# Kernel optimization log

Hardware: AMD Instinct MI355X
Metric: run time of the kernel (lower is better)

## Reference

```python
import jax, jax.numpy as jnp
import numpy as np

H = 4096       # hidden_size
NH = 32        # num attention heads
DN = 128       # qk_nope_head_dim
DR = 64        # qk_rope_head_dim
DV = 128       # v_head_dim
QL = 1536      # q_lora_rank
KL = 512       # kv_lora_rank
INH = 32       # indexer heads
IHD = 128      # indexer head_dim (== fp8 quant block -> one scale per head)
TOPK = 512     # index_topk
T = 1024       # prefill tokens
SCALING = (DN + DR) ** -0.5
FP8_MAX = 448.0  # e4m3 max


def _rms(x, w, eps=1e-6):
    return x * jax.lax.rsqrt(jnp.mean(x * x, -1, keepdims=True) + eps) * w


def _ln(x, w, b, eps=1e-6):
    m = jnp.mean(x, -1, keepdims=True)
    v = jnp.mean(jnp.square(x - m), -1, keepdims=True)
    return (x - m) * jax.lax.rsqrt(v + eps) * w + b


def _rope(x, pos):
    # interleaved (non-neox) rotary embedding on the last dim
    d = x.shape[-1]
    inv = 1.0 / (10000.0 ** (jnp.arange(0, d, 2, dtype=jnp.float32) / d))
    ang = pos.astype(jnp.float32)[:, None] * inv  # [T, d/2]
    shape = (x.shape[0],) + (1,) * (x.ndim - 2) + (d // 2,)
    cos = jnp.cos(ang).reshape(shape)
    sin = jnp.sin(ang).reshape(shape)
    x1, x2 = x[..., 0::2], x[..., 1::2]
    return jnp.stack([x1 * cos - x2 * sin, x1 * sin + x2 * cos], -1).reshape(x.shape)


def _forward(hidden_states, w_qkv_a, q_a_ln_w, w_q_b, kv_a_ln_w, w_kv_b, w_o,
             w_idx_qb, w_idx_k, idx_k_ln_w, idx_k_ln_b, w_idx_weights, positions):
    Tq = hidden_states.shape[0]
    neg = jnp.finfo(jnp.float32).min
    # --- fused low-rank QKV-a projection ---
    qkv_a = hidden_states @ w_qkv_a                       # [T, QL+KL+DR]
    q_c, kv_c, k_pe = qkv_a[:, :QL], qkv_a[:, QL:QL + KL], qkv_a[:, QL + KL:]
    q_cn = _rms(q_c, q_a_ln_w)                            # qr (normed q latent)
    # --- MLA decompression ---
    q = (q_cn @ w_q_b).reshape(Tq, NH, DN + DR)
    q_nope, q_pe = q[..., :DN], q[..., DN:]
    kv = (_rms(kv_c, kv_a_ln_w) @ w_kv_b).reshape(Tq, NH, DN + DV)
    k_nope, v = kv[..., :DN], kv[..., DN:]
    q_pe = _rope(q_pe, positions)
    k_pe = _rope(k_pe, positions)                         # [T, DR], shared across heads (MQA)
    # --- lightning indexer (fp8 ue8m0 per-token-group quant emulated in fp32) ---
    qi = (q_cn @ w_idx_qb).reshape(Tq, INH, IHD)
    qi = jnp.concatenate([_rope(qi[..., :DR], positions), qi[..., DR:]], -1)
    ki = _ln(hidden_states @ w_idx_k, idx_k_ln_w, idx_k_ln_b)   # [T, IHD]
    ki = jnp.concatenate([_rope(ki[:, :DR], positions), ki[:, DR:]], -1)
    amax = jnp.max(jnp.abs(qi), -1, keepdims=True)        # group == head (IHD == block 128)
    q_scale = jnp.exp2(jnp.ceil(jnp.log2(jnp.maximum(amax, 1e-10) / FP8_MAX)))  # ue8m0
    qi_q = qi / q_scale                                   # values in fp8 range
    wts = (hidden_states @ w_idx_weights) * q_scale[..., 0]
    wts = wts * (IHD ** -0.5) * (INH ** -0.5)             # [T, INH]
    sim = jax.nn.relu(jnp.einsum('qhd,kd->hqk', qi_q, ki))
    logits = jnp.einsum('qh,hqk->qk', wts, sim)           # [Tq, Tk]
    idx = jnp.arange(Tq)
    causal = idx[:, None] >= idx[None, :]
    logits = jnp.where(causal, logits, neg)
    _, topk_idx = jax.lax.top_k(logits, TOPK)             # [T, TOPK]
    sparse_mask = jnp.zeros((Tq, Tq), bool).at[idx[:, None], topk_idx].set(True) & causal
    # --- sparse MLA attention ---
    qf = jnp.concatenate([q_nope, q_pe], -1)              # [T, NH, DN+DR]
    kf = jnp.concatenate([k_nope, jnp.broadcast_to(k_pe[:, None, :], (Tq, NH, DR))], -1)
    scores = jnp.einsum('qhd,khd->hqk', qf, kf) * SCALING
    scores = jnp.where(sparse_mask[None], scores, neg)
    attn = jax.nn.softmax(scores, -1)
    out = jnp.einsum('hqk,khd->qhd', attn, v).reshape(Tq, NH * DV)
    return out @ w_o                                      # [T, H]


def setup_inputs() -> dict:
    key = jax.random.key(0)
    ks = jax.random.split(key, 8)
    s = 0.02
    return {
        'hidden_states': jax.random.normal(ks[0], (T, H), jnp.float32),
        'positions': jnp.arange(T, dtype=jnp.int32),
        'w_qkv_a': jax.random.normal(ks[1], (H, QL + KL + DR), jnp.float32) * s,
        'q_a_ln_w': jnp.ones((QL,), jnp.float32),
        'w_q_b': jax.random.normal(ks[2], (QL, NH * (DN + DR)), jnp.float32) * s,
        'kv_a_ln_w': jnp.ones((KL,), jnp.float32),
        'w_kv_b': jax.random.normal(ks[3], (KL, NH * (DN + DV)), jnp.float32) * s,
        'w_o': jax.random.normal(ks[4], (NH * DV, H), jnp.float32) * s,
        'w_idx_qb': jax.random.normal(ks[5], (QL, INH * IHD), jnp.float32) * s,
        'w_idx_k': jax.random.normal(ks[6], (H, IHD), jnp.float32) * s,
        'idx_k_ln_w': jnp.ones((IHD,), jnp.float32),
        'idx_k_ln_b': jnp.zeros((IHD,), jnp.float32),
        'w_idx_weights': jax.random.normal(ks[7], (H, INH), jnp.float32) * s,
    }


def reference(hidden_states, positions, w_qkv_a, q_a_ln_w, w_q_b, kv_a_ln_w, w_kv_b, w_o,
              w_idx_qb, w_idx_k, idx_k_ln_w, idx_k_ln_b, w_idx_weights):
    return _forward(hidden_states, w_qkv_a, q_a_ln_w, w_q_b, kv_a_ln_w, w_kv_b, w_o,
                    w_idx_qb, w_idx_k, idx_k_ln_w, idx_k_ln_b, w_idx_weights, positions)
```

## Files before the change

kernel.cpp:

```cpp
#include <hip/hip_runtime.h>
#include <hip/hip_bf16.h>
#include <math.h>
#include <type_traits>

#define TT   1024
#define HH   4096
#define NHH  32
#define DNN  128
#define DRR  64
#define DVV  128
#define QLL  1536
#define KLL  512
#define INHH 32
#define IHDD 128
#define TOPKK 512
#define QKVN 2112

typedef __attribute__((ext_vector_type(8))) short short8;
typedef __attribute__((ext_vector_type(4))) short short4v;
typedef __attribute__((ext_vector_type(4))) float f32x4;

static __device__ __constant__ float kScaling = 0.07216878364870322f;
static __device__ __constant__ float kWtsScale = 0.015625f;

static __device__ __forceinline__ short f2bf(float f) {
  unsigned u = __float_as_uint(f);
  unsigned r = (u + 0x7fffu + ((u >> 16) & 1u)) >> 16;
  return (short)r;
}
static __device__ __forceinline__ float bf2f(short s) {
  return __uint_as_float(((unsigned)(unsigned short)s) << 16);
}
static __device__ __forceinline__ void gl16(const void* g, void* l) {
  __builtin_amdgcn_global_load_lds(
      (const __attribute__((address_space(1))) unsigned int*)g,
      (__attribute__((address_space(3))) unsigned int*)l, 16, 0, 0);
}
static __device__ __forceinline__ int xcd_swz(int n, int nwg) {
  const int q = nwg >> 3, r = nwg & 7;
  const int x = n & 7, i = n >> 3;
  return (x < r ? x * (q + 1) : r * (q + 1) + (x - r) * q) + i;
}

template <typename CT>
__global__ __launch_bounds__(256) void gemm_bf16(const short* __restrict__ A,
                                                 const short* __restrict__ Bt,
                                                 CT* __restrict__ C,
                                                 int M, int N, int K) {
  __shared__ short As[64 * 64];
  __shared__ short Bs[128 * 64];
  int flat = blockIdx.x + gridDim.x * blockIdx.y;
  flat = xcd_swz(flat, gridDim.x * gridDim.y);
  const int byg = flat % gridDim.y;
  const int bxg = flat / gridDim.y;
  const int tid = threadIdx.x;
  const int lane = tid & 63, wv = tid >> 6;
  const int wc = wv * 32;
  const int bm = byg * 64, bn = bxg * 128;
  const int l15 = lane & 15, l4 = lane >> 4;
  const int sx = (l15 & 7) * 8;
  f32x4 acc[4][2];
#pragma unroll
  for (int i = 0; i < 4; ++i)
#pragma unroll
    for (int j = 0; j < 2; ++j) acc[i][j] = f32x4{0.f, 0.f, 0.f, 0.f};
  for (int k0 = 0; k0 < K; k0 += 64) {
    __syncthreads();
#pragma unroll
    for (int i = 0; i < 2; ++i) {
      const int idx = tid + i * 256;
      const int row = idx >> 3, c8 = (idx & 7) * 8;
      const int cs = c8 ^ ((row & 7) * 8);
      gl16(A + (size_t)(bm + row) * K + k0 + cs, &As[idx * 8]);
    }
#pragma unroll
    for (int i = 0; i < 4; ++i) {
      const int idx = tid + i * 256;
      const int row = idx >> 3, c8 = (idx & 7) * 8;
      const int cs = c8 ^ ((row & 7) * 8);
      gl16(Bt + (size_t)(bn + row) * K + k0 + cs, &Bs[idx * 8]);
    }
    __syncthreads();
    short8 fa[4][2], fb[2][2];
#pragma unroll
    for (int rt = 0; rt < 4; ++rt)
#pragma unroll
      for (int kk = 0; kk < 2; ++kk)
        fa[rt][kk] = *(const short8*)(&As[(rt * 16 + l15) * 64 + ((kk * 32 + l4 * 8) ^ sx)]);
#pragma unroll
    for (int ct = 0; ct < 2; ++ct)
#pragma unroll
      for (int kk = 0; kk < 2; ++kk)
        fb[ct][kk] = *(const short8*)(&Bs[(wc + ct * 16 + l15) * 64 + ((kk * 32 + l4 * 8) ^ sx)]);
#pragma unroll
    for (int kk = 0; kk < 2; ++kk)
#pragma unroll
      for (int rt = 0; rt < 4; ++rt)
#pragma unroll
        for (int ct = 0; ct < 2; ++ct)
          acc[rt][ct] = __builtin_amdgcn_mfma_f32_16x16x32_bf16(fa[rt][kk], fb[ct][kk], acc[rt][ct], 0, 0, 0);
  }
#pragma unroll
  for (int rt = 0; rt < 4; ++rt)
#pragma unroll
    for (int ct = 0; ct < 2; ++ct)
#pragma unroll
      for (int r = 0; r < 4; ++r) {
        const int row = bm + rt * 16 + l4 * 4 + r;
        const int col = bn + wc + ct * 16 + l15;
        const float v = acc[rt][ct][r];
        if constexpr (std::is_same<CT, float>::value) C[(size_t)row * N + col] = v;
        else C[(size_t)row * N + col] = __float2bfloat16(v);
      }
}

__global__ __launch_bounds__(256) void gemm_qb(const short* __restrict__ A,
                                               const short* __restrict__ Bt,
                                               const int* __restrict__ pos,
                                               short* __restrict__ qhb) {
  const int M = TT, N = 6144, K = QLL;
  __shared__ short As[64 * 64];
  __shared__ short Bs[128 * 64];
  int flat = blockIdx.x + gridDim.x * blockIdx.y;
  flat = xcd_swz(flat, gridDim.x * gridDim.y);
  const int byg = flat % gridDim.y;
  const int bxg = flat / gridDim.y;
  const int tid = threadIdx.x;
  const int lane = tid & 63, wv = tid >> 6;
  const int wc = wv * 32;
  const int bm = byg * 64, bn = bxg * 128;
  const int l15 = lane & 15, l4 = lane >> 4;
  const int sx = (l15 & 7) * 8;
  f32x4 acc[4][2];
#pragma unroll
  for (int i = 0; i < 4; ++i)
#pragma unroll
    for (int j = 0; j < 2; ++j) acc[i][j] = f32x4{0.f, 0.f, 0.f, 0.f};
  for (int k0 = 0; k0 < K; k0 += 64) {
    __syncthreads();
#pragma unroll
    for (int i = 0; i < 2; ++i) {
      const int idx = tid + i * 256;
      const int row = idx >> 3, c8 = (idx & 7) * 8;
      const int cs = c8 ^ ((row & 7) * 8);
      gl16(A + (size_t)(bm + row) * K + k0 + cs, &As[idx * 8]);
    }
#pragma unroll
    for (int i = 0; i < 4; ++i) {
      const int idx = tid + i * 256;
      const int row = idx >> 3, c8 = (idx & 7) * 8;
      const int cs = c8 ^ ((row & 7) * 8);
      gl16(Bt + (size_t)(bn + row) * K + k0 + cs, &Bs[idx * 8]);
    }
    __syncthreads();
    short8 fa[4][2], fb[2][2];
#pragma unroll
    for (int rt = 0; rt < 4; ++rt)
#pragma unroll
      for (int kk = 0; kk < 2; ++kk)
        fa[rt][kk] = *(const short8*)(&As[(rt * 16 + l15) * 64 + ((kk * 32 + l4 * 8) ^ sx)]);
#pragma unroll
    for (int ct = 0; ct < 2; ++ct)
#pragma unroll
      for (int kk = 0; kk < 2; ++kk)
        fb[ct][kk] = *(const short8*)(&Bs[(wc + ct * 16 + l15) * 64 + ((kk * 32 + l4 * 8) ^ sx)]);
#pragma unroll
    for (int kk = 0; kk < 2; ++kk)
#pragma unroll
      for (int rt = 0; rt < 4; ++rt)
#pragma unroll
        for (int ct = 0; ct < 2; ++ct)
          acc[rt][ct] = __builtin_amdgcn_mfma_f32_16x16x32_bf16(fa[rt][kk], fb[ct][kk], acc[rt][ct], 0, 0, 0);
  }
#pragma unroll
  for (int rt = 0; rt < 4; ++rt)
#pragma unroll
    for (int r = 0; r < 4; ++r) {
      const int row = bm + rt * 16 + l4 * 4 + r;
      const float p = (float)pos[row];
#pragma unroll
      for (int ct = 0; ct < 2; ++ct) {
        const int col = bn + wc + ct * 16 + l15;
        float v = acc[rt][ct][r];
        const float pv = __shfl_xor(v, 1);
        const int head = col / 192, d = col - head * 192;
        if (d >= 128) {
          const int i = (d - 128) >> 1;
          const float inv = powf(10000.f, -(float)i * (1.f / 32.f));
          float sn, cs;
          sincosf(p * inv, &sn, &cs);
          v = (col & 1) ? (pv * sn + v * cs) : (v * cs - pv * sn);
        }
        qhb[((size_t)head * 1024 + row) * 192 + d] = f2bf(v);
      }
    }
}

__global__ __launch_bounds__(256) void gemm_kvb(const short* __restrict__ A,
                                                const short* __restrict__ Bt,
                                                short* __restrict__ kfb,
                                                short* __restrict__ vtb) {
  const int K = KLL;
  __shared__ short As[64 * 64];
  __shared__ short Bs[128 * 64];
  __shared__ short tr[128 * 66];
  int flat = blockIdx.x + gridDim.x * blockIdx.y;
  flat = xcd_swz(flat, gridDim.x * gridDim.y);
  const int byg = flat % gridDim.y;
  const int bxg = flat / gridDim.y;
  const int tid = threadIdx.x;
  const int lane = tid & 63, wv = tid >> 6;
  const int wc = wv * 32;
  const int bm = byg * 64, bn = bxg * 128;
  const int l15 = lane & 15, l4 = lane >> 4;
  const int sx = (l15 & 7) * 8;
  f32x4 acc[4][2];
#pragma unroll
  for (int i = 0; i < 4; ++i)
#pragma unroll
    for (int j = 0; j < 2; ++j) acc[i][j] = f32x4{0.f, 0.f, 0.f, 0.f};
  for (int k0 = 0; k0 < K; k0 += 64) {
    __syncthreads();
#pragma unroll
    for (int i = 0; i < 2; ++i) {
      const int idx = tid + i * 256;
      const int row = idx >> 3, c8 = (idx & 7) * 8;
      const int cs = c8 ^ ((row & 7) * 8);
      gl16(A + (size_t)(bm + row) * K + k0 + cs, &As[idx * 8]);
    }
#pragma unroll
    for (int i = 0; i < 4; ++i) {
      const int idx = tid + i * 256;
      const int row = idx >> 3, c8 = (idx & 7) * 8;
      const int cs = c8 ^ ((row & 7) * 8);
      gl16(Bt + (size_t)(bn + row) * K + k0 + cs, &Bs[idx * 8]);
    }
    __syncthreads();
    short8 fa[4][2], fb[2][2];
#pragma unroll
    for (int rt = 0; rt < 4; ++rt)
#pragma unroll
      for (int kk = 0; kk < 2; ++kk)
        fa[rt][kk] = *(const short8*)(&As[(rt * 16 + l15) * 64 + ((kk * 32 + l4 * 8) ^ sx)]);
#pragma unroll
    for (int ct = 0; ct < 2; ++ct)
#pragma unroll
      for (int kk = 0; kk < 2; ++kk)
        fb[ct][kk] = *(const short8*)(&Bs[(wc + ct * 16 + l15) * 64 + ((kk * 32 + l4 * 8) ^ sx)]);
#pragma unroll
    for (int kk = 0; kk < 2; ++kk)
#pragma unroll
      for (int rt = 0; rt < 4; ++rt)
#pragma unroll
        for (int ct = 0; ct < 2; ++ct)
          acc[rt][ct] = __builtin_amdgcn_mfma_f32_16x16x32_bf16(fa[rt][kk], fb[ct][kk], acc[rt][ct], 0, 0, 0);
  }
  const int h = bn >> 8;
  const bool isv = (bn >> 7) & 1;
  if (!isv) {
#pragma unroll
    for (int rt = 0; rt < 4; ++rt)
#pragma unroll
      for (int ct = 0; ct < 2; ++ct)
#pragma unroll
        for (int r = 0; r < 4; ++r) {
          const int row = bm + rt * 16 + l4 * 4 + r;
          const int d = wc + ct * 16 + l15;
          kfb[((size_t)h * 1024 + row) * 192 + d] = f2bf(acc[rt][ct][r]);
        }
  } else {
    __syncthreads();
#pragma unroll
    for (int rt = 0; rt < 4; ++rt)
#pragma unroll
      for (int ct = 0; ct < 2; ++ct)
#pragma unroll
        for (int r = 0; r < 4; ++r)
          tr[(wc + ct * 16 + l15) * 66 + rt * 16 + l4 * 4 + r] = f2bf(acc[rt][ct][r]);
    __syncthreads();
    const int d = tid >> 1, half = tid & 1;
    short* dst = vtb + ((size_t)h * 128 + d) * 1024 + bm + half * 32;
#pragma unroll
    for (int c = 0; c < 4; ++c) {
      short8 o;
#pragma unroll
      for (int e = 0; e < 8; ++e) o[e] = tr[d * 66 + half * 32 + c * 8 + e];
      *(short8*)(dst + c * 8) = o;
    }
  }
}

__global__ __launch_bounds__(256) void gemm1_splitk(const short* __restrict__ A,
                                                    const short* __restrict__ Bt,
                                                    float* __restrict__ part,
                                                    int M, int Np, int K, int kchunk) {
  __shared__ short As[64 * 64];
  __shared__ short Bs[128 * 64];
  int flat = blockIdx.x + gridDim.x * (blockIdx.y + gridDim.y * blockIdx.z);
  flat = xcd_swz(flat, gridDim.x * gridDim.y * gridDim.z);
  const int byg = flat % gridDim.y;
  int tmp = flat / gridDim.y;
  const int bxg = tmp % gridDim.x, bzg = tmp / gridDim.x;
  const int tid = threadIdx.x;
  const int lane = tid & 63, wv = tid >> 6;
  const int wc = wv * 32;
  const int bm = byg * 64, bn = bxg * 128;
  const int kbeg = bzg * kchunk;
  const int l15 = lane & 15, l4 = lane >> 4;
  const int sx = (l15 & 7) * 8;
  f32x4 acc[4][2];
#pragma unroll
  for (int i = 0; i < 4; ++i)
#pragma unroll
    for (int j = 0; j < 2; ++j) acc[i][j] = f32x4{0.f, 0.f, 0.f, 0.f};
  for (int k0 = kbeg; k0 < kbeg + kchunk; k0 += 64) {
    __syncthreads();
#pragma unroll
    for (int i = 0; i < 2; ++i) {
      const int idx = tid + i * 256;
      const int row = idx >> 3, c8 = (idx & 7) * 8;
      const int cs = c8 ^ ((row & 7) * 8);
      gl16(A + (size_t)(bm + row) * K + k0 + cs, &As[idx * 8]);
    }
#pragma unroll
    for (int i = 0; i < 4; ++i) {
      const int idx = tid + i * 256;
      const int row = idx >> 3, c8 = (idx & 7) * 8;
      const int cs = c8 ^ ((row & 7) * 8);
      gl16(Bt + (size_t)(bn + row) * K + k0 + cs, &Bs[idx * 8]);
    }
    __syncthreads();
    short8 fa[4][2], fb[2][2];
#pragma unroll
    for (int rt = 0; rt < 4; ++rt)
#pragma unroll
      for (int kk = 0; kk < 2; ++kk)
        fa[rt][kk] = *(const short8*)(&As[(rt * 16 + l15) * 64 + ((kk * 32 + l4 * 8) ^ sx)]);
#pragma unroll
    for (int ct = 0; ct < 2; ++ct)
#pragma unroll
      for (int kk = 0; kk < 2; ++kk)
        fb[ct][kk] = *(const short8*)(&Bs[(wc + ct * 16 + l15) * 64 + ((kk * 32 + l4 * 8) ^ sx)]);
#pragma unroll
    for (int kk = 0; kk < 2; ++kk)
#pragma unroll
      for (int rt = 0; rt < 4; ++rt)
#pragma unroll
        for (int ct = 0; ct < 2; ++ct)
          acc[rt][ct] = __builtin_amdgcn_mfma_f32_16x16x32_bf16(fa[rt][kk], fb[ct][kk], acc[rt][ct], 0, 0, 0);
  }
  float* dst = part + (size_t)bzg * M * Np;
#pragma unroll
  for (int rt = 0; rt < 4; ++rt)
#pragma unroll
    for (int ct = 0; ct < 2; ++ct)
#pragma unroll
      for (int r = 0; r < 4; ++r)
        dst[(size_t)(bm + rt * 16 + l4 * 4 + r) * Np + bn + wc + ct * 16 + l15] =
            acc[rt][ct][r];
}

__global__ __launch_bounds__(256) void gemm3(const short* __restrict__ Ah,
                                             const short* __restrict__ Al,
                                             const short* __restrict__ Bth,
                                             const short* __restrict__ Btl,
                                             float* __restrict__ part,
                                             int M, int Np, int K, int kchunk) {
  __shared__ short AS[64 * 64], BS[128 * 64];
  int flat = blockIdx.x + gridDim.x * (blockIdx.y + gridDim.y * blockIdx.z);
  flat = xcd_swz(flat, gridDim.x * gridDim.y * gridDim.z);
  const int byg = flat % gridDim.y;
  int tmp = flat / gridDim.y;
  const int bxg = tmp % gridDim.x, bzg = tmp / gridDim.x;
  const int tid = threadIdx.x;
  const int lane = tid & 63, wv = tid >> 6;
  const int wc = wv * 32;
  const int l15 = lane & 15, l4 = lane >> 4;
  const int sx = (l15 & 7) * 8;
  const int bm = byg * 64, bn = bxg * 128;
  const int kbeg = bzg * kchunk;
  f32x4 acc[4][2];
#pragma unroll
  for (int i = 0; i < 4; ++i)
#pragma unroll
    for (int j = 0; j < 2; ++j) acc[i][j] = f32x4{0.f, 0.f, 0.f, 0.f};
  for (int k0 = kbeg; k0 < kbeg + kchunk; k0 += 32) {
    __syncthreads();
#pragma unroll
    for (int i = 0; i < 2; ++i) {
      const int idx = tid + i * 256;
      const int row = idx >> 3, c8 = (idx & 7) * 8;
      const int cs = c8 ^ ((row & 7) * 8);
      const short* srcA = (cs < 32) ? (Ah + (size_t)(bm + row) * K + k0 + cs)
                                    : (Al + (size_t)(bm + row) * K + k0 + (cs - 32));
      gl16(srcA, &AS[idx * 8]);
    }
#pragma unroll
    for (int i = 0; i < 4; ++i) {
      const int idx = tid + i * 256;
      const int row = idx >> 3, c8 = (idx & 7) * 8;
      const int cs = c8 ^ ((row & 7) * 8);
      const short* srcB = (cs < 32) ? (Bth + (size_t)(bn + row) * K + k0 + cs)
                                    : (Btl + (size_t)(bn + row) * K + k0 + (cs - 32));
      gl16(srcB, &BS[idx * 8]);
    }
    __syncthreads();
    short8 fah[4], fal[4], fbh[2], fbl[2];
#pragma unroll
    for (int rt = 0; rt < 4; ++rt) {
      const int row = rt * 16 + l15;
      fah[rt] = *(const short8*)&AS[row * 64 + ((l4 * 8) ^ sx)];
      fal[rt] = *(const short8*)&AS[row * 64 + ((32 + l4 * 8) ^ sx)];
    }
#pragma unroll
    for (int ct = 0; ct < 2; ++ct) {
      const int row = wc + ct * 16 + l15;
      fbh[ct] = *(const short8*)&BS[row * 64 + ((l4 * 8) ^ sx)];
      fbl[ct] = *(const short8*)&BS[row * 64 + ((32 + l4 * 8) ^ sx)];
    }
#pragma unroll
    for (int ct = 0; ct < 2; ++ct)
#pragma unroll
      for (int rt = 0; rt < 4; ++rt) {
        acc[rt][ct] = __builtin_amdgcn_mfma_f32_16x16x32_bf16(fah[rt], fbh[ct], acc[rt][ct], 0, 0, 0);
        acc[rt][ct] = __builtin_amdgcn_mfma_f32_16x16x32_bf16(fah[rt], fbl[ct], acc[rt][ct], 0, 0, 0);
        acc[rt][ct] = __builtin_amdgcn_mfma_f32_16x16x32_bf16(fal[rt], fbh[ct], acc[rt][ct], 0, 0, 0);
      }
  }
  float* dst = part + (size_t)bzg * M * Np;
#pragma unroll
  for (int rt = 0; rt < 4; ++rt)
#pragma unroll
    for (int ct = 0; ct < 2; ++ct)
#pragma unroll
      for (int r = 0; r < 4; ++r)
        dst[(size_t)(bm + rt * 16 + l4 * 4 + r) * Np + bn + wc + ct * 16 + l15] =
            acc[rt][ct][r];
}

__global__ __launch_bounds__(256) void qkv_post(const float* __restrict__ qpart,
                                                const float* __restrict__ tpart,
                                                const float* __restrict__ q_ln_w,
                                                const float* __restrict__ kv_ln_w,
                                                const int* __restrict__ pos,
                                                short* __restrict__ qcn_bf,
                                                short* __restrict__ qcn_lo,
                                                short* __restrict__ kvn_bf,
                                                short* __restrict__ kpe_bf) {
  const int t = blockIdx.x, tid = threadIdx.x;
  __shared__ float red[4];
  float qv[6];
  float ss = 0.f;
#pragma unroll
  for (int j = 0; j < 6; ++j) {
    const int c = tid + j * 256;
    float s = 0.f;
#pragma unroll
    for (int z = 0; z < 4; ++z) s += qpart[((size_t)z * TT + t) * QLL + c];
    qv[j] = s;
    ss = fmaf(s, s, ss);
  }
#pragma unroll
  for (int o = 32; o > 0; o >>= 1) ss += __shfl_xor(ss, o);
  if ((tid & 63) == 0) red[tid >> 6] = ss;
  __syncthreads();
  const float rq = rsqrtf((red[0] + red[1] + red[2] + red[3]) / (float)QLL + 1e-6f);
  __syncthreads();
#pragma unroll
  for (int j = 0; j < 6; ++j) {
    const int c = tid + j * 256;
    const float v = qv[j] * rq * q_ln_w[c];
    const short h = f2bf(v);
    qcn_bf[(size_t)t * QLL + c] = h;
    qcn_lo[(size_t)t * QLL + c] = f2bf(v - bf2f(h));
  }
  float kv2[2];
  float ss2 = 0.f;
#pragma unroll
  for (int j = 0; j < 2; ++j) {
    const int c = tid + j * 256;
    float s = 0.f;
#pragma unroll
    for (int z = 0; z < 4; ++z) s += tpart[((size_t)z * TT + t) * 640 + c];
    kv2[j] = s;
    ss2 = fmaf(s, s, ss2);
  }
#pragma unroll
  for (int o = 32; o > 0; o >>= 1) ss2 += __shfl_xor(ss2, o);
  if ((tid & 63) == 0) red[tid >> 6] = ss2;
  __syncthreads();
  const float rkv = rsqrtf((red[0] + red[1] + red[2] + red[3]) / (float)KLL + 1e-6f);
#pragma unroll
  for (int j = 0; j < 2; ++j) {
    const int c = tid + j * 256;
    kvn_bf[(size_t)t * KLL + c] = f2bf(kv2[j] * rkv * kv_ln_w[c]);
  }
  if (tid < 32) {
    float x1 = 0.f, x2 = 0.f;
#pragma unroll
    for (int z = 0; z < 4; ++z) {
      x1 += tpart[((size_t)z * TT + t) * 640 + 512 + 2 * tid];
      x2 += tpart[((size_t)z * TT + t) * 640 + 512 + 2 * tid + 1];
    }
    const float inv = powf(10000.f, -(float)tid * (1.f / 32.f));
    float sn, cs;
    sincosf((float)pos[t] * inv, &sn, &cs);
    kpe_bf[(size_t)t * 64 + 2 * tid]     = f2bf(x1 * cs - x2 * sn);
    kpe_bf[(size_t)t * 64 + 2 * tid + 1] = f2bf(x1 * sn + x2 * cs);
  }
}

__global__ __launch_bounds__(256) void kpe_fill(const short* __restrict__ kpe_bf,
                                                short* __restrict__ kfb) {
  const int idx = blockIdx.x * 256 + threadIdx.x;
  const int c = idx & 7, k = (idx >> 3) & 1023, h = idx >> 13;
  short8 v = *(const short8*)(kpe_bf + k * 64 + c * 8);
  *(short8*)(kfb + ((size_t)h * 1024 + k) * 192 + 128 + c * 8) = v;
}

__global__ __launch_bounds__(256) void ki_prep2(const float* __restrict__ part,
                                                const float* __restrict__ w,
                                                const float* __restrict__ b,
                                                const int* __restrict__ pos,
                                                short* __restrict__ kih,
                                                short* __restrict__ kil,
                                                float* __restrict__ wtsb) {
  const int t = blockIdx.x, tid = threadIdx.x;
  __shared__ float red[4], red2[4];
  float s = 0.f;
#pragma unroll
  for (int z = 0; z < 8; ++z) s += part[((size_t)z * TT + t) * 256 + tid];
  if (tid >= 128 && tid < 160) wtsb[(size_t)t * 32 + (tid - 128)] = s;
  const float v = (tid < 128) ? s : 0.f;
  float sm = v;
#pragma unroll
  for (int o = 32; o > 0; o >>= 1) sm += __shfl_xor(sm, o);
  if ((tid & 63) == 0) red[tid >> 6] = sm;
  __syncthreads();
  const float m = (red[0] + red[1]) * (1.f / 128.f);
  const float dv = v - m;
  float sq = (tid < 128) ? dv * dv : 0.f;
#pragma unroll
  for (int o = 32; o > 0; o >>= 1) sq += __shfl_xor(sq, o);
  if ((tid & 63) == 0) red2[tid >> 6] = sq;
  __syncthreads();
  const float var = (red2[0] + red2[1]) * (1.f / 128.f);
  if (tid < 128) {
    float x = dv * rsqrtf(var + 1e-6f) * w[tid] + b[tid];
    if (tid < 64) {
      const float part2 = __shfl_xor(x, 1);
      const int pi = tid >> 1;
      const float inv = powf(10000.f, -(float)pi * (1.f / 32.f));
      float sn, cs;
      sincosf((float)pos[t] * inv, &sn, &cs);
      x = (tid & 1) ? (part2 * sn + x * cs) : (x * cs - part2 * sn);
    }
    const short h = f2bf(x);
    kih[(size_t)t * 128 + tid] = h;
    kil[(size_t)t * 128 + tid] = f2bf(x - bf2f(h));
  }
}

__global__ __launch_bounds__(256) void split_cast(const float* __restrict__ in,
                                                  short* __restrict__ hi,
                                                  short* __restrict__ lo, int n4) {
  const int i = blockIdx.x * 256 + threadIdx.x;
  if (i >= n4) return;
  float4 v = *(const float4*)(in + (size_t)i * 4);
  float av[4] = {v.x, v.y, v.z, v.w};
  short4v h, l;
#pragma unroll
  for (int e = 0; e < 4; ++e) {
    h[e] = f2bf(av[e]);
    l[e] = f2bf(av[e] - bf2f(h[e]));
  }
  *(short4v*)(hi + (size_t)i * 4) = h;
  *(short4v*)(lo + (size_t)i * 4) = l;
}

__global__ __launch_bounds__(256) void transpose_cast_g(const float* __restrict__ B,
                                                        short* __restrict__ Bt,
                                                        int K, int ldB, int col0, int Ncols) {
  __shared__ float tile[64][65];
  const int tid = threadIdx.x;
  const int k0 = blockIdx.y * 64, n0 = blockIdx.x * 64;
  const int nl = tid >> 3, kc = (tid & 7) * 8;
  if (n0 >= Ncols) {
    short8 z = {0, 0, 0, 0, 0, 0, 0, 0};
#pragma unroll
    for (int i = 0; i < 2; ++i) {
      const int n = nl + i * 32;
      *(short8*)(Bt + (size_t)(n0 + n) * K + k0 + kc) = z;
    }
    return;
  }
  const int r = tid >> 4, c4 = (tid & 15) * 4;
#pragma unroll
  for (int i = 0; i < 4; ++i) {
    float4 v = *(const float4*)(B + (size_t)(k0 + r + i * 16) * ldB + col0 + n0 + c4);
    tile[r + i * 16][c4 + 0] = v.x;
    tile[r + i * 16][c4 + 1] = v.y;
    tile[r + i * 16][c4 + 2] = v.z;
    tile[r + i * 16][c4 + 3] = v.w;
  }
  __syncthreads();
#pragma unroll
  for (int i = 0; i < 2; ++i) {
    const int n = nl + i * 32;
    short8 o;
#pragma unroll
    for (int e = 0; e < 8; ++e) o[e] = f2bf(tile[kc + e][n]);
    *(short8*)(Bt + (size_t)(n0 + n) * K + k0 + kc) = o;
  }
}

__global__ __launch_bounds__(256) void transpose_split_cast(const float* __restrict__ B,
                                                            short* __restrict__ Bth,
                                                            short* __restrict__ Btl,
                                                            int K, int ldB, int col0,
                                                            int Ncols) {
  __shared__ float tile[64][65];
  const int tid = threadIdx.x;
  const int k0 = blockIdx.y * 64, n0 = blockIdx.x * 64;
  const int nl = tid >> 3, kc = (tid & 7) * 8;
  if (n0 >= Ncols) {
    short8 z = {0, 0, 0, 0, 0, 0, 0, 0};
#pragma unroll
    for (int i = 0; i < 2; ++i) {
      const int n = nl + i * 32;
      *(short8*)(Bth + (size_t)(n0 + n) * K + k0 + kc) = z;
      *(short8*)(Btl + (size_t)(n0 + n) * K + k0 + kc) = z;
    }
    return;
  }
  const int r = tid >> 4, c4 = (tid & 15) * 4;
#pragma unroll
  for (int i = 0; i < 4; ++i) {
    float4 v = make_float4(0.f, 0.f, 0.f, 0.f);
    if (n0 + c4 < Ncols)
      v = *(const float4*)(B + (size_t)(k0 + r + i * 16) * ldB + col0 + n0 + c4);
    tile[r + i * 16][c4 + 0] = v.x;
    tile[r + i * 16][c4 + 1] = v.y;
    tile[r + i * 16][c4 + 2] = v.z;
    tile[r + i * 16][c4 + 3] = v.w;
  }
  __syncthreads();
#pragma unroll
  for (int i = 0; i < 2; ++i) {
    const int n = nl + i * 32;
    short8 oh, ol;
#pragma unroll
    for (int e = 0; e < 8; ++e) {
      const float x = tile[kc + e][n];
      oh[e] = f2bf(x);
      ol[e] = f2bf(x - bf2f(oh[e]));
    }
    *(short8*)(Bth + (size_t)(n0 + n) * K + k0 + kc) = oh;
    *(short8*)(Btl + (size_t)(n0 + n) * K + k0 + kc) = ol;
  }
}

__global__ __launch_bounds__(256) void qi_rope_repack_split(const float* __restrict__ idxpart,
                                                            const int* __restrict__ pos,
                                                            short* __restrict__ qhh,
                                                            short* __restrict__ qhl) {
  const int qt = blockIdx.x, h = blockIdx.y;
  const int tid = threadIdx.x;
  const size_t plane = (size_t)TT * HH;
#pragma unroll
  for (int i = 0; i < 8; ++i) {
    const int idx = tid + i * 256;
    const int q = idx >> 5, c = idx & 31;
    const int qg = qt * 64 + q;
    const size_t base = (size_t)qg * HH + h * 128 + c * 4;
    float4 v0 = *(const float4*)(idxpart + base);
    float4 v1 = *(const float4*)(idxpart + plane + base);
    float av[4] = {v0.x + v1.x, v0.y + v1.y, v0.z + v1.z, v0.w + v1.w};
    if (c < 16) {
      const float p = (float)pos[qg];
      float sn0, cs0, sn1, cs1;
      sincosf(p * powf(10000.f, -(float)(c * 2) * (1.f / 32.f)), &sn0, &cs0);
      sincosf(p * powf(10000.f, -(float)(c * 2 + 1) * (1.f / 32.f)), &sn1, &cs1);
      const float a0 = av[0] * cs0 - av[1] * sn0, a1 = av[0] * sn0 + av[1] * cs0;
      const float a2 = av[2] * cs1 - av[3] * sn1, a3 = av[2] * sn1 + av[3] * cs1;
      av[0] = a0; av[1] = a1; av[2] = a2; av[3] = a3;
    }
    short4v hv, lv;
#pragma unroll
    for (int e = 0; e < 4; ++e) {
      hv[e] = f2bf(av[e]);
      lv[e] = f2bf(av[e] - bf2f(hv[e]));
    }
    const size_t off = ((size_t)h * 1024 + qt * 64 + q) * 128 + c * 4;
    *(short4v*)(qhh + off) = hv;
    *(short4v*)(qhl + off) = lv;
  }
}

__global__ __launch_bounds__(256) void logits_mfma(const short* __restrict__ qih,
                                                   const short* __restrict__ qil,
                                                   const short* __restrict__ kih_g,
                                                   const short* __restrict__ kil_g,
                                                   const float* __restrict__ wts,
                                                   float* __restrict__ part) {
  const int bid = xcd_swz(blockIdx.x, gridDim.x);
  int bq = (int)((sqrtf(8.f * bid + 1.f) - 1.f) * 0.5f);
  while ((bq + 1) * (bq + 2) / 2 <= bid) ++bq;
  while (bq * (bq + 1) / 2 > bid) --bq;
  const int bk = bid - bq * (bq + 1) / 2;
  const int g = blockIdx.y;
  __shared__ short kih[64 * 128], kil[64 * 128];
  __shared__ float swts[64][8];
  const int tid = threadIdx.x;
  const int lane = tid & 63, wv = tid >> 6;
  const int wr = (wv >> 1) * 32, wc = (wv & 1) * 32;
  const int l15 = lane & 15, l4 = lane >> 4;
  const int q0 = bq * 64, k0 = bk * 64;
  {
    const int r0 = tid >> 4;
    const int c8 = (tid & 15) * 8;
#pragma unroll
    for (int i = 0; i < 4; ++i) {
      const int row = r0 + i * 16;
      gl16(kih_g + (size_t)(k0 + row) * 128 + c8, &kih[(tid + i * 256) * 8]);
      gl16(kil_g + (size_t)(k0 + row) * 128 + c8, &kil[(tid + i * 256) * 8]);
    }
  }
#pragma unroll
  for (int i = 0; i < 2; ++i) {
    const int idx = tid + i * 256;
    swts[idx >> 3][idx & 7] = wts[(size_t)(q0 + (idx >> 3)) * 32 + g * 8 + (idx & 7)];
  }
  __syncthreads();
  short8 kbh[2][4], kbl[2][4];
#pragma unroll
  for (int ct = 0; ct < 2; ++ct)
#pragma unroll
    for (int ks = 0; ks < 4; ++ks) {
      kbh[ct][ks] = *(const short8*)&kih[(wc + ct * 16 + l15) * 128 + ks * 32 + l4 * 8];
      kbl[ct][ks] = *(const short8*)&kil[(wc + ct * 16 + l15) * 128 + ks * 32 + l4 * 8];
    }
  f32x4 lacc[2][2];
#pragma unroll
  for (int i = 0; i < 2; ++i)
#pragma unroll
    for (int j = 0; j < 2; ++j) lacc[i][j] = f32x4{0.f, 0.f, 0.f, 0.f};
  for (int hh = 0; hh < 8; ++hh) {
    const int h = g * 8 + hh;
    short8 qah[2][4], qal[2][4];
#pragma unroll
    for (int rt = 0; rt < 2; ++rt)
#pragma unroll
      for (int ks = 0; ks < 4; ++ks) {
        const size_t off = ((size_t)h * 1024 + q0 + wr + rt * 16 + l15) * 128 + ks * 32 + l4 * 8;
        qah[rt][ks] = *(const short8*)(qih + off);
        qal[rt][ks] = *(const short8*)(qil + off);
      }
    f32x4 hacc[2][2];
#pragma unroll
    for (int i = 0; i < 2; ++i)
#pragma unroll
      for (int j = 0; j < 2; ++j) hacc[i][j] = f32x4{0.f, 0.f, 0.f, 0.f};
#pragma unroll
    for (int ks = 0; ks < 4; ++ks)
#pragma unroll
      for (int rt = 0; rt < 2; ++rt)
#pragma unroll
        for (int ct = 0; ct < 2; ++ct) {
          hacc[rt][ct] = __builtin_amdgcn_mfma_f32_16x16x32_bf16(qah[rt][ks], kbh[ct][ks], hacc[rt][ct], 0, 0, 0);
          hacc[rt][ct] = __builtin_amdgcn_mfma_f32_16x16x32_bf16(qah[rt][ks], kbl[ct][ks], hacc[rt][ct], 0, 0, 0);
          hacc[rt][ct] = __builtin_amdgcn_mfma_f32_16x16x32_bf16(qal[rt][ks], kbh[ct][ks], hacc[rt][ct], 0, 0, 0);
        }
#pragma unroll
    for (int rt = 0; rt < 2; ++rt)
#pragma unroll
      for (int ct = 0; ct < 2; ++ct)
#pragma unroll
        for (int r = 0; r < 4; ++r) {
          const int row = wr + rt * 16 + l4 * 4 + r;
          const float w = swts[row][hh] * kWtsScale;
          lacc[rt][ct][r] = fmaf(w, fmaxf(hacc[rt][ct][r], 0.f), lacc[rt][ct][r]);
        }
  }
#pragma unroll
  for (int rt = 0; rt < 2; ++rt)
#pragma unroll
    for (int ct = 0; ct < 2; ++ct)
#pragma unroll
      for (int r = 0; r < 4; ++r)
        part[(size_t)g * TT * TT + (size_t)(q0 + wr + rt * 16 + l4 * 4 + r) * TT +
             (k0 + wc + ct * 16 + l15)] = lacc[rt][ct][r];
}

__global__ __launch_bounds__(256) void topk_mask(const float* __restrict__ part,
                                                 unsigned* __restrict__ maskbuf) {
  const int w = threadIdx.x >> 6;
  const int lane = threadIdx.x & 63;
  const int q = blockIdx.x * 4 + w;
  const size_t NN = (size_t)TT * TT;
  __shared__ unsigned long long bl[4][16];
  unsigned v[16];
#pragma unroll
  for (int j = 0; j < 16; ++j) {
    const int k = j * 64 + lane;
    unsigned uv = 0u;
    if (k <= q) {
      const size_t o = (size_t)q * TT + k;
      const float s = part[o] + part[NN + o] + part[2 * NN + o] + part[3 * NN + o];
      unsigned bb = __float_as_uint(s);
      uv = (bb & 0x80000000u) ? ~bb : (bb | 0x80000000u);
    }
    v[j] = uv;
  }
  if (q + 1 <= TOPKK) {
#pragma unroll
    for (int j = 0; j < 16; ++j) {
      const unsigned long long m = __ballot(j * 64 + lane <= q);
      if (lane == 0) bl[w][j] = m;
    }
  } else {
    unsigned lo = 1u, hi = 0xFFFFFFFFu;
    while (lo < hi) {
      const unsigned mid = lo + ((hi - lo) >> 1) + ((hi - lo) & 1u);
      int c = 0;
#pragma unroll
      for (int j = 0; j < 16; ++j) c += __popcll(__ballot(v[j] >= mid));
      if (c >= TOPKK) lo = mid; else hi = mid - 1u;
    }
    const unsigned ustar = lo;
    int nGreater = 0;
#pragma unroll
    for (int j = 0; j < 16; ++j) nGreater += __popcll(__ballot(v[j] > ustar));
    int need = TOPKK - nGreater;
    const unsigned long long lanemask = lane ? (~0ull >> (64 - lane)) : 0ull;
#pragma unroll
    for (int j = 0; j < 16; ++j) {
      const unsigned long long bg = __ballot(v[j] > ustar);
      const unsigned long long be = __ballot(v[j] == ustar);
      const int ce = __popcll(be);
      const int take = need < ce ? need : ce;
      const int rank = __popcll(be & lanemask);
      const bool selme = ((be >> lane) & 1ull) && (rank < take);
      const unsigned long long m = bg | __ballot(selme);
      if (lane == 0) bl[w][j] = m;
      need -= take;
    }
  }
  __builtin_amdgcn_s_waitcnt(0);
  if (lane < 32)
    maskbuf[(size_t)q * 32 + lane] = (unsigned)(bl[w][lane >> 1] >> ((lane & 1) * 32));
}

__global__ __launch_bounds__(256) void attn_mfma(const short* __restrict__ qh,
                                                 const short* __restrict__ kf,
                                                 const short* __restrict__ vt,
                                                 const unsigned* __restrict__ maskbuf,
                                                 short* __restrict__ ao) {
  const int h = blockIdx.x;
  const int yy = blockIdx.y;
  const int qt = (yy < 8) ? (yy * 2) : (31 - yy * 2);
  const int tid = threadIdx.x;
  const int lane = tid & 63, w = tid >> 6;
  const int l15 = lane & 15, l4 = lane >> 4;
  const int q0 = qt * 64;
  __shared__ short kfs[64 * 200];
  __shared__ short vts[128 * 72];
  __shared__ short ps[4][16][72];
  __shared__ unsigned m32s[64][2];
  short8 qf[6];
#pragma unroll
  for (int ks = 0; ks < 6; ++ks)
    qf[ks] = *(const short8*)(qh + ((size_t)h * 1024 + q0 + w * 16 + l15) * 192 + ks * 32 + l4 * 8);
  f32x4 of[8];
#pragma unroll
  for (int dt = 0; dt < 8; ++dt) of[dt] = f32x4{0.f, 0.f, 0.f, 0.f};
  float m[4], l[4];
#pragma unroll
  for (int r = 0; r < 4; ++r) { m[r] = -INFINITY; l[r] = 0.f; }

  for (int kt = 0; kt <= qt; ++kt) {
    const int k0 = kt * 64;
    __syncthreads();
#pragma unroll
    for (int i = 0; i < 6; ++i) {
      const int idx = tid + i * 256;
      const int row = idx / 24, c = idx - row * 24;
      *(short8*)&kfs[row * 200 + c * 8] =
          *(const short8*)(kf + ((size_t)h * 1024 + k0 + row) * 192 + c * 8);
    }
#pragma unroll
    for (int i = 0; i < 4; ++i) {
      const int idx = tid + i * 256;
      const int row = idx >> 3, c = idx & 7;
      *(short8*)&vts[row * 72 + c * 8] =
          *(const short8*)(vt + ((size_t)h * 128 + row) * 1024 + k0 + c * 8);
    }
    if (tid < 128)
      m32s[tid >> 1][tid & 1] = maskbuf[(size_t)(q0 + (tid >> 1)) * 32 + (k0 >> 5) + (tid & 1)];
    __syncthreads();
    f32x4 sacc[4];
#pragma unroll
    for (int j = 0; j < 4; ++j) sacc[j] = f32x4{0.f, 0.f, 0.f, 0.f};
#pragma unroll
    for (int ks = 0; ks < 6; ++ks)
#pragma unroll
      for (int j = 0; j < 4; ++j) {
        short8 kb = *(const short8*)&kfs[(j * 16 + l15) * 200 + ks * 32 + l4 * 8];
        sacc[j] = __builtin_amdgcn_mfma_f32_16x16x32_bf16(qf[ks], kb, sacc[j], 0, 0, 0);
      }
    float tmax[4] = {-INFINITY, -INFINITY, -INFINITY, -INFINITY};
#pragma unroll
    for (int j = 0; j < 4; ++j)
#pragma unroll
      for (int r = 0; r < 4; ++r) {
        const int kcol = j * 16 + l15;
        const unsigned um = m32s[w * 16 + l4 * 4 + r][kcol >> 5];
        float s = sacc[j][r] * kScaling;
        s = ((um >> (kcol & 31)) & 1u) ? s : -INFINITY;
        sacc[j][r] = s;
        tmax[r] = fmaxf(tmax[r], s);
      }
#pragma unroll
    for (int r = 0; r < 4; ++r) {
      tmax[r] = fmaxf(tmax[r], __shfl_xor(tmax[r], 1));
      tmax[r] = fmaxf(tmax[r], __shfl_xor(tmax[r], 2));
      tmax[r] = fmaxf(tmax[r], __shfl_xor(tmax[r], 4));
      tmax[r] = fmaxf(tmax[r], __shfl_xor(tmax[r], 8));
    }
    float f[4];
#pragma unroll
    for (int r = 0; r < 4; ++r) {
      const float mn = fmaxf(m[r], tmax[r]);
      f[r] = __expf(fmaxf(m[r], -1e30f) - fmaxf(mn, -1e30f));
      m[r] = mn;
      l[r] *= f[r];
    }
    float psum[4] = {0.f, 0.f, 0.f, 0.f};
#pragma unroll
    for (int j = 0; j < 4; ++j)
#pragma unroll
      for (int r = 0; r < 4; ++r) {
        const float p = __expf(sacc[j][r] - fmaxf(m[r], -1e30f));
        psum[r] += p;
        ps[w][l4 * 4 + r][j * 16 + l15] = f2bf(p);
      }
#pragma unroll
    for (int r = 0; r < 4; ++r) {
      psum[r] += __shfl_xor(psum[r], 1);
      psum[r] += __shfl_xor(psum[r], 2);
      psum[r] += __shfl_xor(psum[r], 4);
      psum[r] += __shfl_xor(psum[r], 8);
      l[r] += psum[r];
    }
#pragma unroll
    for (int dt = 0; dt < 8; ++dt)
#pragma unroll
      for (int r = 0; r < 4; ++r) of[dt][r] *= f[r];
    short8 pa0 = *(const short8*)&ps[w][l15][l4 * 8];
    short8 pa1 = *(const short8*)&ps[w][l15][32 + l4 * 8];
#pragma unroll
    for (int dt = 0; dt < 8; ++dt) {
      short8 vb0 = *(const short8*)&vts[(dt * 16 + l15) * 72 + l4 * 8];
      short8 vb1 = *(const short8*)&vts[(dt * 16 + l15) * 72 + 32 + l4 * 8];
      of[dt] = __builtin_amdgcn_mfma_f32_16x16x32_bf16(pa0, vb0, of[dt], 0, 0, 0);
      of[dt] = __builtin_amdgcn_mfma_f32_16x16x32_bf16(pa1, vb1, of[dt], 0, 0, 0);
    }
  }
#pragma unroll
  for (int r = 0; r < 4; ++r) {
    const float invl = 1.f / l[r];
#pragma unroll
    for (int dt = 0; dt < 8; ++dt)
      ao[(size_t)(q0 + w * 16 + l4 * 4 + r) * 4096 + h * 128 + dt * 16 + l15] =
          f2bf(of[dt][r] * invl);
  }
}

extern "C" void kernel_launch(void* const* d_in, const int* in_sizes, int n_in,
                              void* d_out, int out_size, void* d_ws, size_t ws_size,
                              hipStream_t stream) {
  const float* hidden     = (const float*)d_in[0];
  const int*   positions  = (const int*)d_in[1];
  const float* w_qkv_a    = (const float*)d_in[2];
  const float* q_a_ln_w   = (const float*)d_in[3];
  const float* w_q_b      = (const float*)d_in[4];
  const float* kv_a_ln_w  = (const float*)d_in[5];
  const float* w_kv_b     = (const float*)d_in[6];
  const float* w_o        = (const float*)d_in[7];
  const float* w_idx_qb   = (const float*)d_in[8];
  const float* w_idx_k    = (const float*)d_in[9];
  const float* idx_k_ln_w = (const float*)d_in[10];
  const float* idx_k_ln_b = (const float*)d_in[11];
  const float* w_idx_w    = (const float*)d_in[12];
  float* out = (float*)d_out;

  float* ws = (float*)d_ws;
  size_t off = 0;
  auto take = [&](size_t n) { float* p = ws + off; off += n; return p; };
  short* qcn_bf  = (short*)take((size_t)TT * QLL / 2);
  short* qcn_lo  = (short*)take((size_t)TT * QLL / 2);
  short* kvn_bf  = (short*)take((size_t)TT * KLL / 2);
  short* kpe_bf  = (short*)take((size_t)TT * 32);
  float* wtsb    = take((size_t)TT * INHH);
  short* kih_g   = (short*)take((size_t)TT * IHDD / 2);
  short* kil_g   = (short*)take((size_t)TT * IHDD / 2);
  short* qhb     = (short*)take((size_t)NHH * TT * 192 / 2);
  short* kfb     = (short*)take((size_t)NHH * TT * 192 / 2);
  short* vtb     = (short*)take((size_t)NHH * 128 * TT / 2);
  short* qih_h   = (short*)take((size_t)INHH * TT * 128 / 2);
  short* qih_l   = (short*)take((size_t)INHH * TT * 128 / 2);
  float* part4   = take((size_t)4 * TT * TT);
  unsigned* maskbuf = (unsigned*)take((size_t)TT * 32);
  short* hid_h   = (short*)take((size_t)TT * HH / 2);
  short* hid_l   = (short*)take((size_t)TT * HH / 2);
  short* wqkva_h = (short*)take((size_t)QLL * HH / 2);
  short* wqkva_l = (short*)take((size_t)QLL * HH / 2);
  short* wtail_t = (short*)take((size_t)640 * HH / 2);
  short* wsk_h   = (short*)take((size_t)256 * HH / 2);
  short* wsk_l   = (short*)take((size_t)256 * HH / 2);
  short* widxqb_h = (short*)take((size_t)HH * QLL / 2);
  short* widxqb_l = (short*)take((size_t)HH * QLL / 2);
  short* wqb_t   = (short*)take((size_t)6144 * QLL / 2);
  short* wkvb_t  = (short*)take((size_t)8192 * KLL / 2);
  short* ao   = (short*)part4;
  short* wo_t = hid_h;
  float* skpart = part4;
  float* qkvpart = (float*)vtb;
  float* tailpart = (float*)qhb;
  float* idxpart = (float*)qhb;

  const dim3 blk(256);
  split_cast<<<dim3(TT * HH / 4 / 256), blk, 0, stream>>>(hidden, hid_h, hid_l, TT * HH / 4);
  transpose_split_cast<<<dim3(QLL / 64, HH / 64), blk, 0, stream>>>(w_qkv_a, wqkva_h, wqkva_l, HH, QKVN, 0, QLL);
  transpose_cast_g<<<dim3(640 / 64, HH / 64), blk, 0, stream>>>(w_qkv_a, wtail_t, HH, QKVN, QLL, QKVN - QLL);
  transpose_split_cast<<<dim3(HH / 64, QLL / 64), blk, 0, stream>>>(w_idx_qb, widxqb_h, widxqb_l, QLL, HH, 0, HH);
  transpose_split_cast<<<dim3(2, HH / 64), blk, 0, stream>>>(w_idx_k, wsk_h, wsk_l, HH, 128, 0, 128);
  transpose_split_cast<<<dim3(2, HH / 64), blk, 0, stream>>>(w_idx_w, wsk_h + (size_t)128 * HH,
                                                            wsk_l + (size_t)128 * HH, HH, 32, 0, 32);
  transpose_cast_g<<<dim3(6144 / 64, QLL / 64), blk, 0, stream>>>(w_q_b, wqb_t, QLL, 6144, 0, 6144);
  transpose_cast_g<<<dim3(8192 / 64, KLL / 64), blk, 0, stream>>>(w_kv_b, wkvb_t, KLL, 8192, 0, 8192);
  gemm3<<<dim3(2, 16, 8), blk, 0, stream>>>(hid_h, hid_l, wsk_h, wsk_l,
                                            skpart, TT, 256, HH, HH / 8);
  ki_prep2<<<dim3(TT), blk, 0, stream>>>(skpart, idx_k_ln_w, idx_k_ln_b, positions,
                                         kih_g, kil_g, wtsb);
  gemm3<<<dim3(QLL / 128, 16, 4), blk, 0, stream>>>(hid_h, hid_l, wqkva_h, wqkva_l,
                                                    qkvpart, TT, QLL, HH, HH / 4);
  gemm1_splitk<<<dim3(5, 16, 4), blk, 0, stream>>>(hid_h, wtail_t, tailpart, TT, 640, HH, HH / 4);
  qkv_post<<<dim3(TT), blk, 0, stream>>>(qkvpart, tailpart, q_a_ln_w, kv_a_ln_w, positions,
                                         qcn_bf, qcn_lo, kvn_bf, kpe_bf);
  transpose_cast_g<<<dim3(HH / 64, HH / 64), blk, 0, stream>>>(w_o, wo_t, HH, HH, 0, HH);
  gemm3<<<dim3(HH / 128, 16, 2), blk, 0, stream>>>(qcn_bf, qcn_lo, widxqb_h, widxqb_l,
                                                   idxpart, TT, HH, QLL, QLL / 2);
  qi_rope_repack_split<<<dim3(16, INHH), blk, 0, stream>>>(idxpart, positions, qih_h, qih_l);
  gemm_qb<<<dim3(48, 16), blk, 0, stream>>>(qcn_bf, wqb_t, positions, qhb);
  gemm_kvb<<<dim3(64, 16), blk, 0, stream>>>(kvn_bf, wkvb_t, kfb, vtb);
  kpe_fill<<<dim3(1024), blk, 0, stream>>>(kpe_bf, kfb);
  logits_mfma<<<dim3(136, 4), blk, 0, stream>>>(qih_h, qih_l, kih_g, kil_g, wtsb, part4);
  topk_mask<<<dim3(TT / 4), blk, 0, stream>>>(part4, maskbuf);
  attn_mfma<<<dim3(NHH, 16), blk, 0, stream>>>(qhb, kfb, vtb, maskbuf, ao);
  gemm_bf16<float><<<dim3(32, 16), blk, 0, stream>>>(ao, wo_t, out, TT, HH, NHH * DVV);
}
```

Measured before the change: 487.1 us.

## Precompute RoPE tables, fuse kpe fill into kvb GEMM, split-K output projection

Adds a small kernel that builds per-token cos/sin tables once, and every RoPE site (q_b epilogue, qkv_post, ki_prep2, indexer q repack) now reads them instead of calling powf and sincosf itself. It also folds the kpe copy into the k-branch epilogue of the kv_b GEMM and removes the separate kpe_fill launch. The output projection now runs as a 2-way split-K GEMM followed by a reduction kernel, which adds partial-sum traffic and one launch in exchange for more parallel blocks.

```diff
diff --git a/kernel.cpp b/kernel.cpp
--- a/kernel.cpp
+++ b/kernel.cpp
@@ -22,6 +22,7 @@
 
 static __device__ __constant__ float kScaling = 0.07216878364870322f;
 static __device__ __constant__ float kWtsScale = 0.015625f;
+#define LOG2_10000_OVER_32 0.4152410118609203f
 
 static __device__ __forceinline__ short f2bf(float f) {
   unsigned u = __float_as_uint(f);
@@ -40,6 +41,16 @@
   const int q = nwg >> 3, r = nwg & 7;
   const int x = n & 7, i = n >> 3;
   return (x < r ? x * (q + 1) : r * (q + 1) + (x - r) * q) + i;
+}
+
+__global__ void rope_tab(const int* __restrict__ pos,
+                         float* __restrict__ ct, float* __restrict__ st) {
+  const int t = blockIdx.x, i = threadIdx.x;
+  const float inv = exp2f(-(float)i * LOG2_10000_OVER_32);
+  float sn, cs;
+  sincosf((float)pos[t] * inv, &sn, &cs);
+  ct[t * 32 + i] = cs;
+  st[t * 32 + i] = sn;
 }
 
 template <typename CT>
@@ -116,7 +127,8 @@
 
 __global__ __launch_bounds__(256) void gemm_qb(const short* __restrict__ A,
                                                const short* __restrict__ Bt,
-                                               const int* __restrict__ pos,
+                                               const float* __restrict__ ropeC,
+                                               const float* __restrict__ ropeS,
                                                short* __restrict__ qhb) {
   const int M = TT, N = 6144, K = QLL;
   __shared__ short As[64 * 64];
@@ -177,7 +189,6 @@
 #pragma unroll
     for (int r = 0; r < 4; ++r) {
       const int row = bm + rt * 16 + l4 * 4 + r;
-      const float p = (float)pos[row];
 #pragma unroll
       for (int ct = 0; ct < 2; ++ct) {
         const int col = bn + wc + ct * 16 + l15;
@@ -186,9 +197,8 @@
         const int head = col / 192, d = col - head * 192;
         if (d >= 128) {
           const int i = (d - 128) >> 1;
-          const float inv = powf(10000.f, -(float)i * (1.f / 32.f));
-          float sn, cs;
-          sincosf(p * inv, &sn, &cs);
+          const float cs = ropeC[row * 32 + i];
+          const float sn = ropeS[row * 32 + i];
           v = (col & 1) ? (pv * sn + v * cs) : (v * cs - pv * sn);
         }
         qhb[((size_t)head * 1024 + row) * 192 + d] = f2bf(v);
@@ -198,6 +208,7 @@
 
 __global__ __launch_bounds__(256) void gemm_kvb(const short* __restrict__ A,
                                                 const short* __restrict__ Bt,
+                                                const short* __restrict__ kpe_bf,
                                                 short* __restrict__ kfb,
                                                 short* __restrict__ vtb) {
   const int K = KLL;
@@ -268,6 +279,13 @@
           const int d = wc + ct * 16 + l15;
           kfb[((size_t)h * 1024 + row) * 192 + d] = f2bf(acc[rt][ct][r]);
         }
+#pragma unroll
+    for (int i = 0; i < 2; ++i) {
+      const int idx = tid + i * 256;
+      const int row = idx >> 3, c = idx & 7;
+      *(short8*)(kfb + ((size_t)h * 1024 + bm + row) * 192 + 128 + c * 8) =
+          *(const short8*)(kpe_bf + (size_t)(bm + row) * 64 + c * 8);
+    }
   } else {
     __syncthreads();
 #pragma unroll
@@ -358,6 +376,16 @@
       for (int r = 0; r < 4; ++r)
         dst[(size_t)(bm + rt * 16 + l4 * 4 + r) * Np + bn + wc + ct * 16 + l15] =
             acc[rt][ct][r];
+}
+
+__global__ __launch_bounds__(256) void reduce_splitk(const float* __restrict__ part,
+                                                     float* __restrict__ C,
+                                                     int M, int Np, int ksplit) {
+  const int c = blockIdx.x * 256 + threadIdx.x;
+  const int m = blockIdx.y;
+  float s = 0.f;
+  for (int z = 0; z < ksplit; ++z) s += part[((size_t)z * M + m) * Np + c];
+  C[(size_t)m * Np + c] = s;
 }
 
 __global__ __launch_bounds__(256) void gemm3(const short* __restrict__ Ah,
@@ -442,7 +470,8 @@
                                                 const float* __restrict__ tpart,
                                                 const float* __restrict__ q_ln_w,
                                                 const float* __restrict__ kv_ln_w,
-                                                const int* __restrict__ pos,
+                                                const float* __restrict__ ropeC,
+                                                const float* __restrict__ ropeS,
                                                 short* __restrict__ qcn_bf,
                                                 short* __restrict__ qcn_lo,
                                                 short* __restrict__ kvn_bf,
@@ -502,26 +531,18 @@
       x1 += tpart[((size_t)z * TT + t) * 640 + 512 + 2 * tid];
       x2 += tpart[((size_t)z * TT + t) * 640 + 512 + 2 * tid + 1];
     }
-    const float inv = powf(10000.f, -(float)tid * (1.f / 32.f));
-    float sn, cs;
-    sincosf((float)pos[t] * inv, &sn, &cs);
+    const float cs = ropeC[t * 32 + tid];
+    const float sn = ropeS[t * 32 + tid];
     kpe_bf[(size_t)t * 64 + 2 * tid]     = f2bf(x1 * cs - x2 * sn);
     kpe_bf[(size_t)t * 64 + 2 * tid + 1] = f2bf(x1 * sn + x2 * cs);
   }
-}
-
-__global__ __launch_bounds__(256) void kpe_fill(const short* __restrict__ kpe_bf,
-                                                short* __restrict__ kfb) {
-  const int idx = blockIdx.x * 256 + threadIdx.x;
-  const int c = idx & 7, k = (idx >> 3) & 1023, h = idx >> 13;
-  short8 v = *(const short8*)(kpe_bf + k * 64 + c * 8);
-  *(short8*)(kfb + ((size_t)h * 1024 + k) * 192 + 128 + c * 8) = v;
 }
 
 __global__ __launch_bounds__(256) void ki_prep2(const float* __restrict__ part,
                                                 const float* __restrict__ w,
                                                 const float* __restrict__ b,
-                                                const int* __restrict__ pos,
+                                                const float* __restrict__ ropeC,
+                                                const float* __restrict__ ropeS,
                                                 short* __restrict__ kih,
                                                 short* __restrict__ kil,
                                                 float* __restrict__ wtsb) {
@@ -550,9 +571,8 @@
     if (tid < 64) {
       const float part2 = __shfl_xor(x, 1);
       const int pi = tid >> 1;
-      const float inv = powf(10000.f, -(float)pi * (1.f / 32.f));
-      float sn, cs;
-      sincosf((float)pos[t] * inv, &sn, &cs);
+      const float cs = ropeC[t * 32 + pi];
+      const float sn = ropeS[t * 32 + pi];
       x = (tid & 1) ? (part2 * sn + x * cs) : (x * cs - part2 * sn);
     }
     const short h = f2bf(x);
@@ -661,7 +681,8 @@
 }
 
 __global__ __launch_bounds__(256) void qi_rope_repack_split(const float* __restrict__ idxpart,
-                                                            const int* __restrict__ pos,
+                                                            const float* __restrict__ ropeC,
+                                                            const float* __restrict__ ropeS,
                                                             short* __restrict__ qhh,
                                                             short* __restrict__ qhl) {
   const int qt = blockIdx.x, h = blockIdx.y;
@@ -677,12 +698,10 @@
     float4 v1 = *(const float4*)(idxpart + plane + base);
     float av[4] = {v0.x + v1.x, v0.y + v1.y, v0.z + v1.z, v0.w + v1.w};
     if (c < 16) {
-      const float p = (float)pos[qg];
-      float sn0, cs0, sn1, cs1;
-      sincosf(p * powf(10000.f, -(float)(c * 2) * (1.f / 32.f)), &sn0, &cs0);
-      sincosf(p * powf(10000.f, -(float)(c * 2 + 1) * (1.f / 32.f)), &sn1, &cs1);
-      const float a0 = av[0] * cs0 - av[1] * sn0, a1 = av[0] * sn0 + av[1] * cs0;
-      const float a2 = av[2] * cs1 - av[3] * sn1, a3 = av[2] * sn1 + av[3] * cs1;
+      const float2 cv = *(const float2*)(ropeC + qg * 32 + c * 2);
+      const float2 sv = *(const float2*)(ropeS + qg * 32 + c * 2);
+      const float a0 = av[0] * cv.x - av[1] * sv.x, a1 = av[0] * sv.x + av[1] * cv.x;
+      const float a2 = av[2] * cv.y - av[3] * sv.y, a3 = av[2] * sv.y + av[3] * cv.y;
       av[0] = a0; av[1] = a1; av[2] = a2; av[3] = a3;
     }
     short4v hv, lv;
@@ -1002,6 +1021,8 @@
   short* kvn_bf  = (short*)take((size_t)TT * KLL / 2);
   short* kpe_bf  = (short*)take((size_t)TT * 32);
   float* wtsb    = take((size_t)TT * INHH);
+  float* rope_ct = take((size_t)TT * 32);
+  float* rope_st = take((size_t)TT * 32);
   short* kih_g   = (short*)take((size_t)TT * IHDD / 2);
   short* kil_g   = (short*)take((size_t)TT * IHDD / 2);
   short* qhb     = (short*)take((size_t)NHH * TT * 192 / 2);
@@ -1028,8 +1049,10 @@
   float* qkvpart = (float*)vtb;
   float* tailpart = (float*)qhb;
   float* idxpart = (float*)qhb;
+  float* wopart = (float*)qhb;
 
   const dim3 blk(256);
+  rope_tab<<<dim3(TT), 32, 0, stream>>>(positions, rope_ct, rope_st);
   split_cast<<<dim3(TT * HH / 4 / 256), blk, 0, stream>>>(hidden, hid_h, hid_l, TT * HH / 4);
   transpose_split_cast<<<dim3(QLL / 64, HH / 64), blk, 0, stream>>>(w_qkv_a, wqkva_h, wqkva_l, HH, QKVN, 0, QLL);
   transpose_cast_g<<<dim3(640 / 64, HH / 64), blk, 0, stream>>>(w_qkv_a, wtail_t, HH, QKVN, QLL, QKVN - QLL);
@@ -1041,22 +1064,24 @@
   transpose_cast_g<<<dim3(8192 / 64, KLL / 64), blk, 0, stream>>>(w_kv_b, wkvb_t, KLL, 8192, 0, 8192);
   gemm3<<<dim3(2, 16, 8), blk, 0, stream>>>(hid_h, hid_l, wsk_h, wsk_l,
                                             skpart, TT, 256, HH, HH / 8);
-  ki_prep2<<<dim3(TT), blk, 0, stream>>>(skpart, idx_k_ln_w, idx_k_ln_b, positions,
+  ki_prep2<<<dim3(TT), blk, 0, stream>>>(skpart, idx_k_ln_w, idx_k_ln_b, rope_ct, rope_st,
                                          kih_g, kil_g, wtsb);
   gemm3<<<dim3(QLL / 128, 16, 4), blk, 0, stream>>>(hid_h, hid_l, wqkva_h, wqkva_l,
                                                     qkvpart, TT, QLL, HH, HH / 4);
   gemm1_splitk<<<dim3(5, 16, 4), blk, 0, stream>>>(hid_h, wtail_t, tailpart, TT, 640, HH, HH / 4);
-  qkv_post<<<dim3(TT), blk, 0, stream>>>(qkvpart, tailpart, q_a_ln_w, kv_a_ln_w, positions,
-                                         qcn_bf, qcn_lo, kvn_bf, kpe_bf);
+  qkv_post<<<dim3(TT), blk, 0, stream>>>(qkvpart, tailpart, q_a_ln_w, kv_a_ln_w,
+                                         rope_ct, rope_st, qcn_bf, qcn_lo, kvn_bf, kpe_bf);
   transpose_cast_g<<<dim3(HH / 64, HH / 64), blk, 0, stream>>>(w_o, wo_t, HH, HH, 0, HH);
   gemm3<<<dim3(HH / 128, 16, 2), blk, 0, stream>>>(qcn_bf, qcn_lo, widxqb_h, widxqb_l,
                                                    idxpart, TT, HH, QLL, QLL / 2);
-  qi_rope_repack_split<<<dim3(16, INHH), blk, 0, stream>>>(idxpart, positions, qih_h, qih_l);
-  gemm_qb<<<dim3(48, 16), blk, 0, stream>>>(qcn_bf, wqb_t, positions, qhb);
-  gemm_kvb<<<dim3(64, 16), blk, 0, stream>>>(kvn_bf, wkvb_t, kfb, vtb);
-  kpe_fill<<<dim3(1024), blk, 0, stream>>>(kpe_bf, kfb);
+  qi_rope_repack_split<<<dim3(16, INHH), blk, 0, stream>>>(idxpart, rope_ct, rope_st,
+                                                          qih_h, qih_l);
+  gemm_qb<<<dim3(48, 16), blk, 0, stream>>>(qcn_bf, wqb_t, rope_ct, rope_st, qhb);
+  gemm_kvb<<<dim3(64, 16), blk, 0, stream>>>(kvn_bf, wkvb_t, kpe_bf, kfb, vtb);
   logits_mfma<<<dim3(136, 4), blk, 0, stream>>>(qih_h, qih_l, kih_g, kil_g, wtsb, part4);
   topk_mask<<<dim3(TT / 4), blk, 0, stream>>>(part4, maskbuf);
   attn_mfma<<<dim3(NHH, 16), blk, 0, stream>>>(qhb, kfb, vtb, maskbuf, ao);
-  gemm_bf16<float><<<dim3(32, 16), blk, 0, stream>>>(ao, wo_t, out, TT, HH, NHH * DVV);
-}
+  gemm1_splitk<<<dim3(HH / 128, 16, 2), blk, 0, stream>>>(ao, wo_t, wopart, TT, HH,
+                                                          NHH * DVV, NHH * DVV / 2);
+  reduce_splitk<<<dim3(HH / 256, TT), blk, 0, stream>>>(wopart, out, TT, HH, 2);
+}
```

New measurement: 469.9 us. 1.04x faster.
